# Kernel optimization log

Measured on AMD Instinct MI355X. Metric: run time of the kernel, lower is better.

Reference implementation:

```python
import jax, jax.numpy as jnp
import numpy as np

B, Tin, Tout = 256, 32, 29
Venc, Vdec = 29, 72
E = 256; H = 256; L = 3; G = 4 * H; D = 2 * L  # bidirectional dirs * layers


def lstm_step(x, h, c, Wih0, Wih1, Whh, b):
    """One timestep of a 3-layer bidirectional LSTM (torch gate order i,f,g,o).
    x: [B, in], h/c: [D, B, H] in torch layout (layer-major, dir-minor)."""
    new_h, new_c = [], []
    inp = x
    for l in range(L):
        outs = []
        for d in range(2):
            idx = 2 * l + d
            Wih = Wih0[d] if l == 0 else Wih1[l - 1, d]
            g = inp @ Wih.T + h[idx] @ Whh[l, d].T + b[l, d]
            i_g, f_g, g_g, o_g = jnp.split(g, 4, axis=-1)
            cc = jax.nn.sigmoid(f_g) * c[idx] + jax.nn.sigmoid(i_g) * jnp.tanh(g_g)
            hh = jax.nn.sigmoid(o_g) * jnp.tanh(cc)
            new_h.append(hh); new_c.append(cc); outs.append(hh)
        inp = jnp.concatenate(outs, axis=-1)  # feeds next layer: [B, 2H]
    return jnp.stack(new_h), jnp.stack(new_c), inp


def proj(hid, W1, b1, W2, b2):
    """Linear over hidden dim then Linear over the layer*dir dim -- the exact
    math of torch's linear1 -> permute(2,1,0) -> linear2 -> permute(2,1,0)."""
    hn = jnp.einsum('lbh,gh->lbg', hid, W1) + b1            # [D, B, H]
    return jnp.einsum('lbh,ml->mbh', hn, W2) + b2[:, None, None]


def setup_inputs() -> dict:
    key = jax.random.key(0)
    ks = iter(jax.random.split(key, 64))
    def p(shape, scale=0.06):
        return jax.random.normal(next(ks), shape, jnp.float32) * scale
    return {
        "input": jax.random.randint(next(ks), (B, Tin), 0, Venc),
        "target": jax.random.randint(next(ks), (B, Tout), 0, Vdec),
        "teacher_force": 1,
        "enc_emb": p((Venc, E)), "dec_emb": p((Vdec, E)),
        "enc_Wih0": p((2, G, E)), "enc_Wih1": p((L - 1, 2, G, 2 * H)),
        "enc_Whh": p((L, 2, G, H)), "enc_b": p((L, 2, G)),
        "dec_Wih0": p((2, G, E)), "dec_Wih1": p((L - 1, 2, G, 2 * H)),
        "dec_Whh": p((L, 2, G, H)), "dec_b": p((L, 2, G)),
        "lin_h_W1": p((H, H)), "lin_h_b1": p((H,)), "lin_h_W2": p((D, D)), "lin_h_b2": p((D,)),
        "lin_c_W1": p((H, H)), "lin_c_b1": p((H,)), "lin_c_W2": p((D, D)), "lin_c_b2": p((D,)),
        "lin_a_W1": p((H, H)), "lin_a_b1": p((H,)), "lin_a_W2": p((D, D)), "lin_a_b2": p((D,)),
        "attn_W": p((E, E + H)), "attn_b": p((E,)),
        "fc_W": p((Vdec, 2 * H)), "fc_b": p((Vdec,)),
    }


def reference(input, target, teacher_force, enc_emb, dec_emb, enc_Wih0, enc_Wih1, enc_Whh, enc_b, dec_Wih0, dec_Wih1, dec_Whh, dec_b, lin_h_W1, lin_h_b1, lin_h_W2, lin_h_b2, lin_c_W1, lin_c_b1, lin_c_W2, lin_c_b2, lin_a_W1, lin_a_b1, lin_a_W2, lin_a_b2, attn_W, attn_b, fc_W, fc_b):
    Bb = input.shape[0]
    h0 = jnp.zeros((D, Bb, H), jnp.float32)

    # ---- encoder: step LSTM over Tin, projecting hidden per step for attention ----
    def enc_step(carry, x_t):
        h, c = carry
        h, c, _ = lstm_step(enc_emb[x_t], h, c, enc_Wih0, enc_Wih1, enc_Whh, enc_b)
        return (h, c), proj(h, lin_a_W1, lin_a_b1, lin_a_W2, lin_a_b2)

    (h, c), encoder_outputs = jax.lax.scan(enc_step, (h0, h0), input.T)  # [Tin, D, B, H]

    # ---- encoder->decoder state bridging (linear over H, linear over D) ----
    dec_h = proj(h, lin_h_W1, lin_h_b1, lin_h_W2, lin_h_b2)
    dec_c = proj(c, lin_c_W1, lin_c_b1, lin_c_W2, lin_c_b2)

    def dec_core(h, c, tok):
        emb = dec_emb[tok]                                # [B, E]
        energies = h[None] * encoder_outputs              # [Tin, D, B, H]
        aw = jax.nn.softmax(energies, axis=0)             # attn over source time
        ctx = (aw * encoder_outputs).sum(0).mean(0)       # [B, H]
        x = jnp.concatenate([emb, ctx], -1) @ attn_W.T + attn_b
        h, c, top = lstm_step(x, h, c, dec_Wih0, dec_Wih1, dec_Whh, dec_b)
        return h, c, top @ fc_W.T + fc_b, aw.sum(-1)      # logits [B,V], aw [Tin,D,B]

    if teacher_force:
        def step(carry, tok):
            h, c = carry
            h, c, logits, _ = dec_core(h, c, tok)
            return (h, c), logits
        _, logits_seq = jax.lax.scan(step, (dec_h, dec_c), target[:, :Tout - 1].T)
        attn_seq = jnp.zeros((Tout - 1, Tin, D, Bb), jnp.float32)
    else:
        def step(carry, _):
            h, c, tok = carry
            h, c, logits, aw = dec_core(h, c, tok)
            nxt = jnp.argmax(jax.nn.softmax(logits, -1), -1).astype(tok.dtype)
            return (h, c, nxt), (logits, aw)
        tok0 = jnp.ones((Bb,), input.dtype)
        _, (logits_seq, attn_seq) = jax.lax.scan(step, (dec_h, dec_c, tok0), None, length=Tout - 1)

    pred0 = jnp.zeros((1, Bb, Vdec), jnp.float32).at[0, :, 1].set(1.0)
    predicted = jnp.concatenate([pred0, logits_seq], 0)   # [Tout, B, Vdec]
    attn_weights = jnp.concatenate([jnp.zeros((1, Tin, D, Bb), jnp.float32), attn_seq], 0)
    return predicted, attn_weights
```

## Files before the change

kernel.cpp:

```cpp
#include <hip/hip_runtime.h>
#include <math.h>

#define BB 256
#define TIN 32
#define TOUT 29
#define VDEC 72
#define EDIM 256
#define HDIM 256
#define DD 6
#define BH (BB*HDIM)
#define NBLK 256

typedef unsigned short u16;
typedef unsigned int u32;
typedef __bf16 bf16x8 __attribute__((ext_vector_type(8)));
typedef float f32x4 __attribute__((ext_vector_type(4)));
typedef u16 u16x8 __attribute__((ext_vector_type(8)));

__device__ __forceinline__ float sigmf(float x){ return 1.0f/(1.0f+__expf(-x)); }
__device__ __forceinline__ float tanhf_fast(float x){ return 1.0f - 2.0f/(1.0f+__expf(2.0f*x)); }
__device__ __forceinline__ u16 f2bf(float f){
  u32 u = __builtin_bit_cast(u32, f);
  u32 r = (u + 0x7fffu + ((u>>16)&1u)) >> 16;
  return (u16)r;
}
__device__ __forceinline__ float bf2f(u16 s){
  u32 u = ((u32)s)<<16; return __builtin_bit_cast(float, u);
}
__device__ __forceinline__ bf16x8 ldbf8(const u16* p){
  u16x8 t = *(const u16x8*)p; return __builtin_bit_cast(bf16x8, t);
}
__device__ __forceinline__ bf16x8 ldbf8v(const u16* p){
  u16x8 t = *(const volatile u16x8*)p; return __builtin_bit_cast(bf16x8, t);
}
__device__ __forceinline__ float ldbfv(const u16* p){ return bf2f(*(const volatile u16*)p); }
__device__ __forceinline__ float ldfv(const float* p){ return *(const volatile float*)p; }
__device__ __forceinline__ f32x4 mfma16(bf16x8 a, bf16x8 b, f32x4 c){
  return __builtin_amdgcn_mfma_f32_16x16x32_bf16(a, b, c, 0, 0, 0);
}

struct GmS { float As[32][33]; float Ws[256][34]; };
union SharedU {
  struct { float Gt[2][4][32][18]; } st;
  GmS gm2[2];
  struct { float s[512]; float p4[VDEC][4]; float lg[VDEC]; float ctxp[2][256]; int tok; } fc;
};

__device__ __forceinline__ void xbar(u32* barblk, int mt, u32 g, int bid, bool fast){
  __syncthreads();
  if (fast){
    u32* cnt  = barblk + 384 + mt*32;
    u32* genx = cnt + 16;
    if (threadIdx.x == 0){
      u32 old = __hip_atomic_fetch_add(cnt, 1u, __ATOMIC_RELAXED, __HIP_MEMORY_SCOPE_AGENT);
      if (old == 31u){
        __hip_atomic_store(cnt, 0u, __ATOMIC_RELAXED, __HIP_MEMORY_SCOPE_AGENT);
        __hip_atomic_store(genx, g, __ATOMIC_RELEASE, __HIP_MEMORY_SCOPE_AGENT);
      } else {
        while (__hip_atomic_load(genx, __ATOMIC_RELAXED, __HIP_MEMORY_SCOPE_AGENT) < g)
          __builtin_amdgcn_s_sleep(2);
      }
    }
    __syncthreads();
  } else {
    u32* arr = barblk;
    u32* gen = barblk + 320;
    if (threadIdx.x == 0)
      __hip_atomic_store(&arr[bid], g, __ATOMIC_RELEASE, __HIP_MEMORY_SCOPE_AGENT);
    if (bid == 0){
      if (threadIdx.x < 256)
        while (__hip_atomic_load(&arr[threadIdx.x], __ATOMIC_RELAXED, __HIP_MEMORY_SCOPE_AGENT) < g)
          __builtin_amdgcn_s_sleep(2);
      __syncthreads();
      if (threadIdx.x == 0)
        __hip_atomic_store(gen, g, __ATOMIC_RELEASE, __HIP_MEMORY_SCOPE_AGENT);
    } else if (threadIdx.x == 0){
      while (__hip_atomic_load(gen, __ATOMIC_RELAXED, __HIP_MEMORY_SCOPE_AGENT) < g)
        __builtin_amdgcn_s_sleep(2);
    }
    __builtin_amdgcn_fence(__ATOMIC_ACQUIRE, "agent");
    __syncthreads();
  }
}

__global__ void fill_zero_u32(u32* __restrict__ p, int n){
  int i = blockIdx.x*256 + threadIdx.x;
  if (i < n) p[i] = 0u;
}

__global__ void init_out_kernel(float* __restrict__ out, int n){
  int i = blockIdx.x*256 + threadIdx.x;
  if (i >= n) return;
  float v = 0.0f;
  if (i < BB*VDEC && (i % VDEC) == 1) v = 1.0f;
  out[i] = v;
}

__global__ void bias2d_kernel(const float* __restrict__ W2a, const float* __restrict__ b1a, const float* __restrict__ b2a,
                              const float* __restrict__ W2h, const float* __restrict__ b1h, const float* __restrict__ b2h,
                              const float* __restrict__ W2c, const float* __restrict__ b1c, const float* __restrict__ b2c,
                              float* __restrict__ outp){
  int g = threadIdx.x;
  const float* W2[3] = {W2a, W2h, W2c};
  const float* b1[3] = {b1a, b1h, b1c};
  const float* b2[3] = {b2a, b2h, b2c};
  for (int p = 0; p < 3; p++)
    for (int m = 0; m < 6; m++){
      float s = 0.f;
      for (int l = 0; l < 6; l++) s += W2[p][m*6+l];
      outp[p*1536 + m*256 + g] = s * b1[p][g] + b2[p][m];
    }
}

__global__ void embed_enc_kernel(const int* __restrict__ input, const float* __restrict__ enc_emb,
                                 u16* __restrict__ x_emb){
  int i = blockIdx.x*256 + threadIdx.x;
  int e = i & 255, b = (i >> 8) & 255, t = i >> 16;
  x_emb[i] = f2bf(enc_emb[(size_t)input[b*TIN + t]*EDIM + e]);
}

__global__ void pack_w_kernel(const float* __restrict__ Wih, const float* __restrict__ Whh,
                              u16* __restrict__ dst, int K1, int K){
  int k = blockIdx.x*256 + threadIdx.x;
  int row = blockIdx.y;
  int d = row >> 10, rr = row & 1023;
  int ht = rr >> 6, r = rr & 63;
  int g = (r>>4)*256 + ht*16 + (r&15);
  float v;
  if (k < K1) v = Wih[((size_t)d*1024 + g)*K1 + k];
  else        v = Whh[((size_t)d*1024 + g)*256 + (k - K1)];
  dst[(size_t)row*K + k] = f2bf(v);
}

__global__ void pack_wfused_kernel(const float* __restrict__ Wih0, const float* __restrict__ attn_W,
                                   const float* __restrict__ Whh, u16* __restrict__ dst){
  int k = blockIdx.x*256 + threadIdx.x;
  int row = blockIdx.y;
  int d = row >> 10, rr = row & 1023;
  int ht = rr >> 6, r = rr & 63;
  int g = (r>>4)*256 + ht*16 + (r&15);
  float v;
  if (k >= 512) v = Whh[((size_t)d*1024 + g)*256 + (k - 512)];
  else {
    const float* wr = Wih0 + ((size_t)d*1024 + g)*256;
    float s = 0.f;
    #pragma unroll 4
    for (int o = 0; o < 256; o++) s += wr[o] * attn_W[(size_t)o*512 + k];
    v = s;
  }
  dst[(size_t)row*768 + k] = f2bf(v);
}

__global__ void biasfold_kernel(const float* __restrict__ Wih0, const float* __restrict__ attn_b,
                                const float* __restrict__ dec_b, float* __restrict__ outb){
  int i = blockIdx.x*256 + threadIdx.x;
  int d = i >> 10, g = i & 1023;
  const float* wr = Wih0 + ((size_t)d*1024 + g)*256;
  float s = dec_b[d*1024 + g];
  #pragma unroll 4
  for (int o = 0; o < 256; o++) s += wr[o]*attn_b[o];
  outb[i] = s;
}

template<int K1>
__device__ __forceinline__ void stage_phase(SharedU* shp, int mt, int y,
    const u16* __restrict__ inp, const u16* __restrict__ Wpk, const float* __restrict__ bias_l,
    const u16* __restrict__ hR, u16* __restrict__ hW, float* __restrict__ cBuf,
    u16* __restrict__ inp_out, float* __restrict__ h_all_t, int l){
  auto& ss = shp->st;
  constexpr int K = K1 + 256;
  constexpr int HK = K/2;
  int tid = threadIdx.x;
  int m_base = mt*32;
  int d = y >> 4, ht = y & 15;
  int idx = 2*l + d;
  int q8 = tid >> 6, lane = tid & 63;
  int qg = q8 & 3, kh2 = q8 >> 2;
  int r = lane & 15, lq = lane >> 4;
  const u16* a0p = inp + (size_t)(m_base + r)*K1 + lq*8;
  const u16* a1p = a0p + (size_t)16*K1;
  const u16* h0p = hR + (size_t)idx*BH + (size_t)(m_base + r)*HDIM + lq*8;
  const u16* h1p = h0p + 16*HDIM;
  const u16* wp  = Wpk + (size_t)((d*16+ht)*64 + qg*16 + r)*K + lq*8;
  const int cbase = kh2*HK;
  f32x4 acc0 = {0.f,0.f,0.f,0.f}, acc1 = {0.f,0.f,0.f,0.f};
  #pragma unroll
  for (int c = 0; c < HK; c += 32){
    int col = cbase + c;
    bool ina = (col < K1);
    const u16* pa0 = ina ? (a0p + col) : (h0p + (col - K1));
    const u16* pa1 = ina ? (a1p + col) : (h1p + (col - K1));
    bf16x8 a0 = ldbf8v(pa0);
    bf16x8 a1 = ldbf8v(pa1);
    bf16x8 bq = ldbf8(wp + col);
    acc0 = mfma16(a0, bq, acc0);
    acc1 = mfma16(a1, bq, acc1);
  }
  __syncthreads();
  #pragma unroll
  for (int rr = 0; rr < 4; rr++){
    ss.Gt[kh2][qg][lq*4 + rr][r]      = acc0[rr];
    ss.Gt[kh2][qg][16 + lq*4 + rr][r] = acc1[rr];
  }
  __syncthreads();
  const float* bias = bias_l + d*1024;
  {
    int bb = tid >> 4, h2 = tid & 15;
    int b = m_base + bb, h = ht*16 + h2;
    float iv = ss.Gt[0][0][bb][h2] + ss.Gt[1][0][bb][h2] + bias[h];
    float fv = ss.Gt[0][1][bb][h2] + ss.Gt[1][1][bb][h2] + bias[256 + h];
    float gv = ss.Gt[0][2][bb][h2] + ss.Gt[1][2][bb][h2] + bias[512 + h];
    float ov = ss.Gt[0][3][bb][h2] + ss.Gt[1][3][bb][h2] + bias[768 + h];
    size_t off = (size_t)idx*BH + (size_t)b*HDIM + h;
    float cold = cBuf[off];
    float cc = sigmf(fv)*cold + sigmf(iv)*tanhf_fast(gv);
    float hv = sigmf(ov)*tanhf_fast(cc);
    cBuf[off] = cc;
    u16 hb = f2bf(hv);
    hW[off] = hb;
    if (inp_out) inp_out[(size_t)b*512 + d*HDIM + h] = hb;
    if (h_all_t) h_all_t[off] = hv;
  }
}

__device__ __forceinline__ void mix_one(int b, int h, const float* __restrict__ inp,
    float* __restrict__ outp, const float* __restrict__ W2, int t){
  size_t base2 = ((size_t)t*6)*BH + (size_t)b*256 + h;
  float v[6];
  #pragma unroll
  for (int l = 0; l < 6; l++) v[l] = ldfv(&inp[base2 + (size_t)l*BH]);
  #pragma unroll
  for (int m = 0; m < 6; m++){
    float s = 0.f;
    #pragma unroll
    for (int l = 0; l < 6; l++) s += W2[m*6+l]*v[l];
    outp[base2 + (size_t)m*BH] = s;
  }
}

__device__ __forceinline__ void gemm_tile(GmS& sg, int tid, int m_base,
    const float* __restrict__ A, float* __restrict__ C, const float* __restrict__ W,
    const float* __restrict__ bias2d, u16* __restrict__ Cbf){
  int rg = tid >> 5, cg = tid & 31;
  float acc[4][8];
  #pragma unroll
  for (int i=0;i<4;i++)
    #pragma unroll
    for (int j=0;j<8;j++) acc[i][j]=0.f;
  for (int k0 = 0; k0 < 256; k0 += 32){
    #pragma unroll
    for (int p=0;p<4;p++) sg.As[rg + p*8][cg] = ldfv(&A[(size_t)(m_base + rg + p*8)*256 + k0 + cg]);
    #pragma unroll
    for (int p=0;p<32;p++) sg.Ws[rg + p*8][cg] = W[(size_t)(rg + p*8)*256 + k0 + cg];
    __syncthreads();
    #pragma unroll
    for (int kk=0; kk<32; kk++){
      float a[4], w[8];
      #pragma unroll
      for (int i=0;i<4;i++) a[i] = sg.As[rg*4+i][kk];
      #pragma unroll
      for (int j=0;j<8;j++) w[j] = sg.Ws[cg + 32*j][kk];
      #pragma unroll
      for (int i=0;i<4;i++)
        #pragma unroll
        for (int j=0;j<8;j++) acc[i][j] += a[i]*w[j];
    }
    __syncthreads();
  }
  #pragma unroll
  for (int i=0;i<4;i++){
    int row = m_base + rg*4 + i;
    int bm = (row >> 8) % 6;
    #pragma unroll
    for (int j=0;j<8;j++){
      int col = cg + 32*j;
      float v = acc[i][j] + bias2d[bm*256 + col];
      if (C)   C[(size_t)row*256 + col] = v;
      if (Cbf) Cbf[(size_t)row*256 + col] = f2bf(v);
    }
  }
}

__device__ __forceinline__ void attn_phase(SharedU* shp, int b, int step,
    const u16* __restrict__ hR, const u16* __restrict__ eo, u16* __restrict__ cat,
    const int* __restrict__ tf, float* __restrict__ attn_out,
    const int* __restrict__ target, float* __restrict__ outp,
    const float* __restrict__ dec_emb, const u16* __restrict__ top,
    const float* __restrict__ fc_W, const float* __restrict__ fc_b){
  auto& sf = shp->fc;
  int tid = threadIdx.x;
  if (step > 0){
    sf.s[tid] = ldbfv(&top[(size_t)b*512 + tid]);
    __syncthreads();
    if (tid < 4*VDEC){
      int v = tid >> 2, part = tid & 3;
      int k0 = part*128;
      const float* wr = fc_W + (size_t)v*512;
      float a = 0.f;
      #pragma unroll 4
      for (int k = k0; k < k0+128; k++) a += sf.s[k]*wr[k];
      sf.p4[v][part] = a;
    }
    __syncthreads();
    if (tid < VDEC){
      float a = fc_b[tid] + sf.p4[tid][0] + sf.p4[tid][1] + sf.p4[tid][2] + sf.p4[tid][3];
      outp[((size_t)step*BB + b)*VDEC + tid] = a;
      sf.lg[tid] = a;
    }
    __syncthreads();
  }
  int tok;
  if (tf[0]) tok = target[b*TOUT + step];
  else if (step == 0) tok = 1;
  else {
    if (tid == 0){
      int bi = 0; float bv = sf.lg[0];
      for (int v = 1; v < VDEC; v++){ float x = sf.lg[v]; if (x > bv){ bv = x; bi = v; } }
      sf.tok = bi;
    }
    __syncthreads();
    tok = sf.tok;
  }
  if (tid < 256) cat[(size_t)b*512 + tid] = f2bf(dec_emb[(size_t)tok*EDIM + tid]);
  int hc = tid & 255, dhalf = tid >> 8;
  bool wa = (tf[0] == 0);
  float acc = 0.f;
  for (int dd = 0; dd < 3; dd++){
    int d = dhalf*3 + dd;
    float hv = ldbfv(&hR[(size_t)d*BH + (size_t)b*256 + hc]);
    const u16* ep = eo + (size_t)d*BH + (size_t)b*256 + hc;
    float se = 0.f, ac = 0.f;
    #pragma unroll 8
    for (int t = 0; t < TIN; t++){
      float ev = bf2f(ep[(size_t)t*(DD*BH)]);
      float e = __expf(hv*ev);
      se += e; ac += e*ev;
    }
    acc += ac/se;
    if (wa){
      float inv = 1.f/se;
      for (int t = 0; t < TIN; t++){
        float ev = bf2f(ep[(size_t)t*(DD*BH)]);
        atomicAdd(&attn_out[(((size_t)(step+1)*TIN + t)*DD + d)*BB + b], __expf(hv*ev)*inv);
      }
    }
  }
  sf.ctxp[dhalf][hc] = acc;
  __syncthreads();
  if (tid < 256)
    cat[(size_t)b*512 + 256 + tid] = f2bf((sf.ctxp[0][tid] + sf.ctxp[1][tid])*(1.0f/6.0f));
}

__device__ __forceinline__ void fc_final_phase(SharedU* shp, int b,
    const u16* __restrict__ top, const float* __restrict__ fc_W,
    const float* __restrict__ fc_b, float* __restrict__ outp){
  auto& sf = shp->fc;
  int tid = threadIdx.x;
  sf.s[tid] = ldbfv(&top[(size_t)b*512 + tid]);
  __syncthreads();
  if (tid < 4*VDEC){
    int v = tid >> 2, part = tid & 3;
    int k0 = part*128;
    const float* wr = fc_W + (size_t)v*512;
    float a = 0.f;
    #pragma unroll 4
    for (int k = k0; k < k0+128; k++) a += sf.s[k]*wr[k];
    sf.p4[v][part] = a;
  }
  __syncthreads();
  if (tid < VDEC){
    float a = fc_b[tid] + sf.p4[tid][0] + sf.p4[tid][1] + sf.p4[tid][2] + sf.p4[tid][3];
    outp[((size_t)(TOUT-1)*BB + b)*VDEC + tid] = a;
  }
}

__global__ __launch_bounds__(512, 2) void mega_kernel(
    const int* __restrict__ target, const int* __restrict__ tf,
    const float* __restrict__ dec_emb, const u16* __restrict__ x_emb,
    const u16* __restrict__ wp_e0, const u16* __restrict__ wp_e1, const u16* __restrict__ wp_e2,
    const u16* __restrict__ wp_d0f, const u16* __restrict__ wp_d1, const u16* __restrict__ wp_d2,
    const float* __restrict__ enc_b, const float* __restrict__ dec_b, const float* __restrict__ fb0,
    const float* __restrict__ lin_h_W1, const float* __restrict__ lin_c_W1, const float* __restrict__ lin_a_W1,
    const float* __restrict__ lin_h_W2, const float* __restrict__ lin_c_W2, const float* __restrict__ lin_a_W2,
    const float* __restrict__ bias2d,
    const float* __restrict__ fc_W, const float* __restrict__ fc_b,
    float* __restrict__ out,
    float* __restrict__ h_all, float* __restrict__ tmp6, float* __restrict__ tmp6c,
    float* __restrict__ dec_c, u16* __restrict__ enc_hA, float* __restrict__ enc_c,
    u16* __restrict__ enc_hB, u16* __restrict__ dec_hA, u16* __restrict__ dec_hB,
    u16* __restrict__ bufA, u16* __restrict__ bufB, u16* __restrict__ cat,
    u16* __restrict__ eo_bf, u32* __restrict__ barblk)
{
  __shared__ SharedU sh;
  __shared__ u32 ord_sh;
  const int bid = blockIdx.x, tid = threadIdx.x;
  u32* ctr = barblk + 336;
  u32* badflag = barblk + 352;
  u32 g = 0;

  u32 xcc;
  asm volatile("s_getreg_b32 %0, hwreg(HW_REG_XCC_ID)" : "=s"(xcc));
  xcc &= 7u;
  if (tid == 0){
    u32 o = __hip_atomic_fetch_add(&ctr[xcc], 1u, __ATOMIC_RELAXED, __HIP_MEMORY_SCOPE_AGENT);
    ord_sh = o;
    if (o >= 32u)
      __hip_atomic_store(badflag, 1u, __ATOMIC_RELAXED, __HIP_MEMORY_SCOPE_AGENT);
  }
  xbar(barblk, 0, ++g, bid, false);
  bool fast = (__hip_atomic_load(badflag, __ATOMIC_RELAXED, __HIP_MEMORY_SCOPE_AGENT) == 0u);
  int mt, y;
  if (fast){ mt = (int)xcc; y = (int)ord_sh; }
  else     { mt = bid & 7;  y = bid >> 3;    }
  const int half = tid >> 8, htid = tid & 255;
  const int b = mt*32 + y;

  for (int t = 0; t < TIN; t++){
    const u16* hRb = (t & 1) ? enc_hB : enc_hA;
    u16*       hWb = (t & 1) ? enc_hA : enc_hB;
    float* hat = h_all + (size_t)t*DD*BH;
    stage_phase<256>(&sh, mt, y, x_emb + (size_t)t*BB*EDIM, wp_e0, enc_b,        hRb, hWb, enc_c, bufA, hat, 0);
    xbar(barblk, mt, ++g, bid, fast);
    stage_phase<512>(&sh, mt, y, bufA,                      wp_e1, enc_b + 2048, hRb, hWb, enc_c, bufB, hat, 1);
    xbar(barblk, mt, ++g, bid, fast);
    stage_phase<512>(&sh, mt, y, bufB,                      wp_e2, enc_b + 4096, hRb, hWb, enc_c, nullptr, hat, 2);
  }
  xbar(barblk, mt, ++g, bid, fast);

  {
    if (half == 0) mix_one(b, htid, h_all + (size_t)31*DD*BH, tmp6,  lin_h_W2, 0);
    else           mix_one(b, htid, enc_c,                    tmp6c, lin_c_W2, 0);
    __syncthreads();
    for (int t2 = half*16; t2 < half*16 + 16; t2++)
      mix_one(b, htid, h_all, h_all, lin_a_W2, t2);
  }
  xbar(barblk, mt, ++g, bid, fast);
  if (y < 6){
    if (half == 0) gemm_tile(sh.gm2[0], htid, y*256 + mt*32, tmp6,  nullptr, lin_h_W1, bias2d + 1536, dec_hA);
    else           gemm_tile(sh.gm2[1], htid, y*256 + mt*32, tmp6c, dec_c,   lin_c_W1, bias2d + 3072, nullptr);
  }
  #pragma unroll
  for (int jj = 0; jj < 3; jj++){
    int k2 = y*6 + half*3 + jj;
    gemm_tile(sh.gm2[half], htid, k2*256 + mt*32, h_all, nullptr, lin_a_W1, bias2d, eo_bf);
  }
  xbar(barblk, mt, ++g, bid, fast);

  float* attn_out = out + (size_t)TOUT*BB*VDEC;
  for (int i = 0; i < TOUT-1; i++){
    const u16* hRb = (i & 1) ? dec_hB : dec_hA;
    u16*       hWb = (i & 1) ? dec_hA : dec_hB;
    attn_phase(&sh, b, i, hRb, eo_bf, cat, tf, attn_out, target, out, dec_emb, bufA, fc_W, fc_b);
    xbar(barblk, mt, ++g, bid, fast);
    stage_phase<512>(&sh, mt, y, cat,  wp_d0f, fb0,          hRb, hWb, dec_c, bufA, nullptr, 0);
    xbar(barblk, mt, ++g, bid, fast);
    stage_phase<512>(&sh, mt, y, bufA, wp_d1,  dec_b + 2048, hRb, hWb, dec_c, bufB, nullptr, 1);
    xbar(barblk, mt, ++g, bid, fast);
    stage_phase<512>(&sh, mt, y, bufB, wp_d2,  dec_b + 4096, hRb, hWb, dec_c, bufA, nullptr, 2);
    xbar(barblk, mt, ++g, bid, fast);
  }
  fc_final_phase(&sh, b, bufA, fc_W, fc_b, out);
}


extern "C" void kernel_launch(void* const* d_in, const int* in_sizes, int n_in,
                              void* d_out, int out_size, void* d_ws, size_t ws_size,
                              hipStream_t stream){
  (void)in_sizes; (void)n_in; (void)out_size; (void)ws_size;
  const int*   input    = (const int*)d_in[0];
  const int*   target   = (const int*)d_in[1];
  const int*   tf       = (const int*)d_in[2];
  const float* enc_emb  = (const float*)d_in[3];
  const float* dec_emb  = (const float*)d_in[4];
  const float* enc_Wih0 = (const float*)d_in[5];
  const float* enc_Wih1 = (const float*)d_in[6];
  const float* enc_Whh  = (const float*)d_in[7];
  const float* enc_b    = (const float*)d_in[8];
  const float* dec_Wih0 = (const float*)d_in[9];
  const float* dec_Wih1 = (const float*)d_in[10];
  const float* dec_Whh  = (const float*)d_in[11];
  const float* dec_b    = (const float*)d_in[12];
  const float* lin_h_W1 = (const float*)d_in[13];
  const float* lin_h_b1 = (const float*)d_in[14];
  const float* lin_h_W2 = (const float*)d_in[15];
  const float* lin_h_b2 = (const float*)d_in[16];
  const float* lin_c_W1 = (const float*)d_in[17];
  const float* lin_c_b1 = (const float*)d_in[18];
  const float* lin_c_W2 = (const float*)d_in[19];
  const float* lin_c_b2 = (const float*)d_in[20];
  const float* lin_a_W1 = (const float*)d_in[21];
  const float* lin_a_b1 = (const float*)d_in[22];
  const float* lin_a_W2 = (const float*)d_in[23];
  const float* lin_a_b2 = (const float*)d_in[24];
  const float* attn_W   = (const float*)d_in[25];
  const float* attn_b   = (const float*)d_in[26];
  const float* fc_W     = (const float*)d_in[27];
  const float* fc_b     = (const float*)d_in[28];
  float* out = (float*)d_out;

  char* base = (char*)d_ws;
  size_t off = 0;
  auto alloc = [&](size_t bytes)->char*{
    char* p = base + off; off += (bytes + 255) & ~(size_t)255; return p;
  };
  float* h_all  = (float*)alloc(sizeof(float)*(size_t)TIN*DD*BH);
  float* tmp6   = (float*)alloc(sizeof(float)*(size_t)DD*BH);
  float* tmp6c  = (float*)alloc(sizeof(float)*(size_t)DD*BH);
  float* dec_c  = (float*)alloc(sizeof(float)*(size_t)DD*BH);
  float* bias2d = (float*)alloc(sizeof(float)*3*6*256);
  u16*   enc_hA = (u16*)alloc(sizeof(u16)*(size_t)DD*BH + sizeof(float)*(size_t)DD*BH);
  float* enc_c  = (float*)(enc_hA + (size_t)DD*BH);
  u16* enc_hB = (u16*)alloc(sizeof(u16)*(size_t)DD*BH);
  u16* dec_hA = (u16*)alloc(sizeof(u16)*(size_t)DD*BH);
  u16* dec_hB = (u16*)alloc(sizeof(u16)*(size_t)DD*BH);
  u16* x_emb  = (u16*)alloc(sizeof(u16)*(size_t)TIN*BB*EDIM);
  u16* bufA   = (u16*)alloc(sizeof(u16)*(size_t)BB*512);
  u16* bufB   = (u16*)alloc(sizeof(u16)*(size_t)BB*512);
  u16* cat    = (u16*)alloc(sizeof(u16)*(size_t)BB*512);
  u16* eo_bf  = (u16*)alloc(sizeof(u16)*(size_t)TIN*DD*BH);
  u16* wp_e0  = (u16*)alloc(sizeof(u16)*(size_t)2048*512);
  u16* wp_e1  = (u16*)alloc(sizeof(u16)*(size_t)2048*768);
  u16* wp_e2  = (u16*)alloc(sizeof(u16)*(size_t)2048*768);
  u16* wp_d0f = (u16*)alloc(sizeof(u16)*(size_t)2048*768);
  u16* wp_d1  = (u16*)alloc(sizeof(u16)*(size_t)2048*768);
  u16* wp_d2  = (u16*)alloc(sizeof(u16)*(size_t)2048*768);
  float* fb0  = (float*)alloc(sizeof(float)*2048);
  u32* barblk = (u32*)alloc(sizeof(u32)*1024);

  const int outn = TOUT*BB*VDEC + TOUT*TIN*DD*BB;
  init_out_kernel<<<(outn+255)/256, 256, 0, stream>>>(out, outn);
  fill_zero_u32<<<(DD*BH*6/4 + 255)/256, 256, 0, stream>>>((u32*)enc_hA, DD*BH*6/4);
  fill_zero_u32<<<4, 256, 0, stream>>>(barblk, 1024);
  bias2d_kernel<<<1, 256, 0, stream>>>(lin_a_W2, lin_a_b1, lin_a_b2,
                                       lin_h_W2, lin_h_b1, lin_h_b2,
                                       lin_c_W2, lin_c_b1, lin_c_b2, bias2d);
  embed_enc_kernel<<<(TIN*BB*EDIM)/256, 256, 0, stream>>>(input, enc_emb, x_emb);
  pack_w_kernel<<<dim3(2,2048), 256, 0, stream>>>(enc_Wih0, enc_Whh,                       wp_e0, 256, 512);
  pack_w_kernel<<<dim3(3,2048), 256, 0, stream>>>(enc_Wih1, enc_Whh + 2*1024*256,          wp_e1, 512, 768);
  pack_w_kernel<<<dim3(3,2048), 256, 0, stream>>>(enc_Wih1 + (size_t)2*1024*512, enc_Whh + 4*1024*256, wp_e2, 512, 768);
  pack_wfused_kernel<<<dim3(3,2048), 256, 0, stream>>>(dec_Wih0, attn_W, dec_Whh,          wp_d0f);
  biasfold_kernel<<<8, 256, 0, stream>>>(dec_Wih0, attn_b, dec_b, fb0);
  pack_w_kernel<<<dim3(3,2048), 256, 0, stream>>>(dec_Wih1, dec_Whh + 2*1024*256,          wp_d1, 512, 768);
  pack_w_kernel<<<dim3(3,2048), 256, 0, stream>>>(dec_Wih1 + (size_t)2*1024*512, dec_Whh + 4*1024*256, wp_d2, 512, 768);

  mega_kernel<<<NBLK, 512, 0, stream>>>(
      target, tf, dec_emb, x_emb,
      wp_e0, wp_e1, wp_e2, wp_d0f, wp_d1, wp_d2,
      enc_b, dec_b, fb0,
      lin_h_W1, lin_c_W1, lin_a_W1, lin_h_W2, lin_c_W2, lin_a_W2,
      bias2d, fc_W, fc_b, out,
      h_all, tmp6, tmp6c, dec_c, enc_hA, enc_c, enc_hB, dec_hA, dec_hB,
      bufA, bufB, cat, eo_bf, barblk);
}
```

Measured before the change: 3.896 ms.

## Run encoder layers as per-block full-sequence passes with state kept in LDS

The encoder is restructured so that each of 32 worker blocks owns one direction and one 16-row batch tile and runs all 32 timesteps of a layer alone. The recurrent hidden state lives in shared memory and the cell state in registers. This replaces the roughly 96 grid-wide barriers per encoder pass with three layer-level barriers. The fast barrier is also rewritten to use a monotonic counter with no reset, and its sleep interval is shortened. The trade-off is that only 32 of 256 blocks do encoder work, and each re-streams its weight slice from L2 every timestep.

```diff
diff --git a/kernel.cpp b/kernel.cpp
--- a/kernel.cpp
+++ b/kernel.cpp
@@ -42,45 +42,45 @@
 struct GmS { float As[32][33]; float Ws[256][34]; };
 union SharedU {
   struct { float Gt[2][4][32][18]; } st;
+  struct { u16 hprev[16][264]; } enc;
   GmS gm2[2];
   struct { float s[512]; float p4[VDEC][4]; float lg[VDEC]; float ctxp[2][256]; int tok; } fc;
 };
 
-__device__ __forceinline__ void xbar(u32* barblk, int mt, u32 g, int bid, bool fast){
-  __syncthreads();
-  if (fast){
-    u32* cnt  = barblk + 384 + mt*32;
-    u32* genx = cnt + 16;
-    if (threadIdx.x == 0){
-      u32 old = __hip_atomic_fetch_add(cnt, 1u, __ATOMIC_RELAXED, __HIP_MEMORY_SCOPE_AGENT);
-      if (old == 31u){
-        __hip_atomic_store(cnt, 0u, __ATOMIC_RELAXED, __HIP_MEMORY_SCOPE_AGENT);
-        __hip_atomic_store(genx, g, __ATOMIC_RELEASE, __HIP_MEMORY_SCOPE_AGENT);
-      } else {
-        while (__hip_atomic_load(genx, __ATOMIC_RELAXED, __HIP_MEMORY_SCOPE_AGENT) < g)
-          __builtin_amdgcn_s_sleep(2);
-      }
-    }
-    __syncthreads();
-  } else {
-    u32* arr = barblk;
-    u32* gen = barblk + 320;
+__device__ __forceinline__ void bar_slow(u32* barblk, u32 gs, int bid){
+  __syncthreads();
+  u32* arr = barblk;
+  u32* gen = barblk + 320;
+  if (threadIdx.x == 0)
+    __hip_atomic_store(&arr[bid], gs, __ATOMIC_RELEASE, __HIP_MEMORY_SCOPE_AGENT);
+  if (bid == 0){
+    if (threadIdx.x < 256)
+      while (__hip_atomic_load(&arr[threadIdx.x], __ATOMIC_RELAXED, __HIP_MEMORY_SCOPE_AGENT) < gs)
+        __builtin_amdgcn_s_sleep(8);
+    __syncthreads();
     if (threadIdx.x == 0)
-      __hip_atomic_store(&arr[bid], g, __ATOMIC_RELEASE, __HIP_MEMORY_SCOPE_AGENT);
-    if (bid == 0){
-      if (threadIdx.x < 256)
-        while (__hip_atomic_load(&arr[threadIdx.x], __ATOMIC_RELAXED, __HIP_MEMORY_SCOPE_AGENT) < g)
-          __builtin_amdgcn_s_sleep(2);
-      __syncthreads();
-      if (threadIdx.x == 0)
-        __hip_atomic_store(gen, g, __ATOMIC_RELEASE, __HIP_MEMORY_SCOPE_AGENT);
-    } else if (threadIdx.x == 0){
-      while (__hip_atomic_load(gen, __ATOMIC_RELAXED, __HIP_MEMORY_SCOPE_AGENT) < g)
-        __builtin_amdgcn_s_sleep(2);
-    }
-    __builtin_amdgcn_fence(__ATOMIC_ACQUIRE, "agent");
-    __syncthreads();
-  }
+      __hip_atomic_store(gen, gs, __ATOMIC_RELEASE, __HIP_MEMORY_SCOPE_AGENT);
+  } else if (threadIdx.x == 0){
+    while (__hip_atomic_load(gen, __ATOMIC_RELAXED, __HIP_MEMORY_SCOPE_AGENT) < gs)
+      __builtin_amdgcn_s_sleep(8);
+  }
+  __builtin_amdgcn_fence(__ATOMIC_ACQUIRE, "agent");
+  __syncthreads();
+}
+
+__device__ __forceinline__ void bar_fast(u32* barblk, int mt, u32 gf){
+  __syncthreads();
+  u32* cnt  = barblk + 384 + mt*32;
+  u32* genx = cnt + 16;
+  if (threadIdx.x == 0){
+    u32 old = __hip_atomic_fetch_add(cnt, 1u, __ATOMIC_RELAXED, __HIP_MEMORY_SCOPE_AGENT);
+    if (old == gf*32u - 1u)
+      __hip_atomic_store(genx, gf, __ATOMIC_RELAXED, __HIP_MEMORY_SCOPE_AGENT);
+    else
+      while (__hip_atomic_load(genx, __ATOMIC_RELAXED, __HIP_MEMORY_SCOPE_AGENT) < gf)
+        __builtin_amdgcn_s_sleep(1);
+  }
+  __syncthreads();
 }
 
 __global__ void fill_zero_u32(u32* __restrict__ p, int n){
@@ -163,10 +163,81 @@
 }
 
 template<int K1>
-__device__ __forceinline__ void stage_phase(SharedU* shp, int mt, int y,
+__device__ __forceinline__ void enc_pass(SharedU* shp, int m0, int d,
+    const u16* __restrict__ g0, const u16* __restrict__ g1, size_t gtstride,
+    const u16* __restrict__ Wpk, const float* __restrict__ bias_d,
+    u16* __restrict__ hseq_p, float* __restrict__ hall_p, float* __restrict__ encc_p){
+  constexpr int K = K1 + 256;
+  const int tid = threadIdx.x;
+  const int wv = tid >> 6, lane = tid & 63;
+  const int r = lane & 15, lq = lane >> 4;
+  for (int i = tid; i < 16*264; i += 512) ((u16*)shp->enc.hprev)[i] = 0;
+  __syncthreads();
+  const u16* wrow[8];
+  #pragma unroll
+  for (int ht2 = 0; ht2 < 2; ht2++)
+    #pragma unroll
+    for (int q = 0; q < 4; q++)
+      wrow[ht2*4+q] = Wpk + (size_t)((d*16 + wv*2 + ht2)*64 + q*16 + r)*K + lq*8;
+  float c8[8];
+  #pragma unroll
+  for (int i = 0; i < 8; i++) c8[i] = 0.f;
+  const int mb = lq*4;
+  #pragma unroll 1
+  for (int t = 0; t < TIN; t++){
+    f32x4 acc[8];
+    #pragma unroll
+    for (int i = 0; i < 8; i++) acc[i] = (f32x4){0.f,0.f,0.f,0.f};
+    #pragma unroll
+    for (int k0 = 0; k0 < K; k0 += 32){
+      bf16x8 a;
+      if (k0 < K1){
+        const u16* gp = (K1 == 512 && k0 >= 256) ? g1 : g0;
+        a = ldbf8v(gp + (size_t)t*gtstride + (size_t)(m0 + r)*256 + (k0 & 255) + lq*8);
+      } else {
+        a = ldbf8(&shp->enc.hprev[r][(k0 - K1) + lq*8]);
+      }
+      #pragma unroll
+      for (int i = 0; i < 8; i++)
+        acc[i] = mfma16(a, ldbf8(wrow[i] + k0), acc[i]);
+    }
+    __syncthreads();
+    #pragma unroll
+    for (int ht2 = 0; ht2 < 2; ht2++){
+      int h = (wv*2 + ht2)*16 + r;
+      #pragma unroll
+      for (int reg = 0; reg < 4; reg++){
+        float iv = acc[ht2*4+0][reg] + bias_d[h];
+        float fv = acc[ht2*4+1][reg] + bias_d[256 + h];
+        float gv = acc[ht2*4+2][reg] + bias_d[512 + h];
+        float ov = acc[ht2*4+3][reg] + bias_d[768 + h];
+        float co = c8[ht2*4+reg];
+        float cc = sigmf(fv)*co + sigmf(iv)*tanhf_fast(gv);
+        float hv = sigmf(ov)*tanhf_fast(cc);
+        c8[ht2*4+reg] = cc;
+        u16 hb = f2bf(hv);
+        shp->enc.hprev[mb + reg][h] = hb;
+        size_t go = (size_t)(m0 + mb + reg)*256 + h;
+        hseq_p[(size_t)t*(DD*BH) + go] = hb;
+        hall_p[(size_t)t*(DD*BH) + go] = hv;
+      }
+    }
+    __syncthreads();
+  }
+  #pragma unroll
+  for (int ht2 = 0; ht2 < 2; ht2++){
+    int h = (wv*2 + ht2)*16 + r;
+    #pragma unroll
+    for (int reg = 0; reg < 4; reg++)
+      encc_p[(size_t)(m0 + mb + reg)*256 + h] = c8[ht2*4+reg];
+  }
+}
+
+template<int K1>
+__device__ __forceinline__ void stage_dec(SharedU* shp, int mt, int y,
     const u16* __restrict__ inp, const u16* __restrict__ Wpk, const float* __restrict__ bias_l,
     const u16* __restrict__ hR, u16* __restrict__ hW, float* __restrict__ cBuf,
-    u16* __restrict__ inp_out, float* __restrict__ h_all_t, int l){
+    u16* __restrict__ inp_out, int l){
   auto& ss = shp->st;
   constexpr int K = K1 + 256;
   constexpr int HK = K/2;
@@ -203,8 +274,8 @@
     ss.Gt[kh2][qg][16 + lq*4 + rr][r] = acc1[rr];
   }
   __syncthreads();
-  const float* bias = bias_l + d*1024;
   {
+    const float* bias = bias_l + d*1024;
     int bb = tid >> 4, h2 = tid & 15;
     int b = m_base + bb, h = ht*16 + h2;
     float iv = ss.Gt[0][0][bb][h2] + ss.Gt[1][0][bb][h2] + bias[h];
@@ -219,7 +290,6 @@
     u16 hb = f2bf(hv);
     hW[off] = hb;
     if (inp_out) inp_out[(size_t)b*512 + d*HDIM + h] = hb;
-    if (h_all_t) h_all_t[off] = hv;
   }
 }
 
@@ -386,8 +456,8 @@
     const float* __restrict__ fc_W, const float* __restrict__ fc_b,
     float* __restrict__ out,
     float* __restrict__ h_all, float* __restrict__ tmp6, float* __restrict__ tmp6c,
-    float* __restrict__ dec_c, u16* __restrict__ enc_hA, float* __restrict__ enc_c,
-    u16* __restrict__ enc_hB, u16* __restrict__ dec_hA, u16* __restrict__ dec_hB,
+    float* __restrict__ dec_c, float* __restrict__ enc_c,
+    u16* __restrict__ hseq, u16* __restrict__ dec_hA, u16* __restrict__ dec_hB,
     u16* __restrict__ bufA, u16* __restrict__ bufB, u16* __restrict__ cat,
     u16* __restrict__ eo_bf, u32* __restrict__ barblk)
 {
@@ -396,7 +466,7 @@
   const int bid = blockIdx.x, tid = threadIdx.x;
   u32* ctr = barblk + 336;
   u32* badflag = barblk + 352;
-  u32 g = 0;
+  u32 gs = 0, gf = 0;
 
   u32 xcc;
   asm volatile("s_getreg_b32 %0, hwreg(HW_REG_XCC_ID)" : "=s"(xcc));
@@ -407,7 +477,7 @@
     if (o >= 32u)
       __hip_atomic_store(badflag, 1u, __ATOMIC_RELAXED, __HIP_MEMORY_SCOPE_AGENT);
   }
-  xbar(barblk, 0, ++g, bid, false);
+  ++gs; bar_slow(barblk, gs, bid);
   bool fast = (__hip_atomic_load(badflag, __ATOMIC_RELAXED, __HIP_MEMORY_SCOPE_AGENT) == 0u);
   int mt, y;
   if (fast){ mt = (int)xcc; y = (int)ord_sh; }
@@ -415,17 +485,25 @@
   const int half = tid >> 8, htid = tid & 255;
   const int b = mt*32 + y;
 
-  for (int t = 0; t < TIN; t++){
-    const u16* hRb = (t & 1) ? enc_hB : enc_hA;
-    u16*       hWb = (t & 1) ? enc_hA : enc_hB;
-    float* hat = h_all + (size_t)t*DD*BH;
-    stage_phase<256>(&sh, mt, y, x_emb + (size_t)t*BB*EDIM, wp_e0, enc_b,        hRb, hWb, enc_c, bufA, hat, 0);
-    xbar(barblk, mt, ++g, bid, fast);
-    stage_phase<512>(&sh, mt, y, bufA,                      wp_e1, enc_b + 2048, hRb, hWb, enc_c, bufB, hat, 1);
-    xbar(barblk, mt, ++g, bid, fast);
-    stage_phase<512>(&sh, mt, y, bufB,                      wp_e2, enc_b + 4096, hRb, hWb, enc_c, nullptr, hat, 2);
-  }
-  xbar(barblk, mt, ++g, bid, fast);
+  bool worker; int wdir, wtile;
+  if (fast){ worker = (y < 4); wdir = mt >> 2; wtile = (mt & 3)*4 + y; }
+  else     { worker = (bid < 32); wdir = bid >> 4; wtile = bid & 15; }
+  const int m0 = wtile*16;
+
+  if (worker)
+    enc_pass<256>(&sh, m0, wdir, x_emb, x_emb, (size_t)BH, wp_e0, enc_b + wdir*1024,
+                  hseq + (size_t)(0+wdir)*BH, h_all + (size_t)(0+wdir)*BH, enc_c + (size_t)(0+wdir)*BH);
+  ++gs; bar_slow(barblk, gs, bid);
+  if (worker)
+    enc_pass<512>(&sh, m0, wdir, hseq + 0*(size_t)BH, hseq + 1*(size_t)BH, (size_t)(DD*BH),
+                  wp_e1, enc_b + 2048 + wdir*1024,
+                  hseq + (size_t)(2+wdir)*BH, h_all + (size_t)(2+wdir)*BH, enc_c + (size_t)(2+wdir)*BH);
+  ++gs; bar_slow(barblk, gs, bid);
+  if (worker)
+    enc_pass<512>(&sh, m0, wdir, hseq + 2*(size_t)BH, hseq + 3*(size_t)BH, (size_t)(DD*BH),
+                  wp_e2, enc_b + 4096 + wdir*1024,
+                  hseq + (size_t)(4+wdir)*BH, h_all + (size_t)(4+wdir)*BH, enc_c + (size_t)(4+wdir)*BH);
+  ++gs; bar_slow(barblk, gs, bid);
 
   {
     if (half == 0) mix_one(b, htid, h_all + (size_t)31*DD*BH, tmp6,  lin_h_W2, 0);
@@ -434,7 +512,7 @@
     for (int t2 = half*16; t2 < half*16 + 16; t2++)
       mix_one(b, htid, h_all, h_all, lin_a_W2, t2);
   }
-  xbar(barblk, mt, ++g, bid, fast);
+  if (fast){ ++gf; bar_fast(barblk, mt, gf); } else { ++gs; bar_slow(barblk, gs, bid); }
   if (y < 6){
     if (half == 0) gemm_tile(sh.gm2[0], htid, y*256 + mt*32, tmp6,  nullptr, lin_h_W1, bias2d + 1536, dec_hA);
     else           gemm_tile(sh.gm2[1], htid, y*256 + mt*32, tmp6c, dec_c,   lin_c_W1, bias2d + 3072, nullptr);
@@ -444,20 +522,20 @@
     int k2 = y*6 + half*3 + jj;
     gemm_tile(sh.gm2[half], htid, k2*256 + mt*32, h_all, nullptr, lin_a_W1, bias2d, eo_bf);
   }
-  xbar(barblk, mt, ++g, bid, fast);
+  if (fast){ ++gf; bar_fast(barblk, mt, gf); } else { ++gs; bar_slow(barblk, gs, bid); }
 
   float* attn_out = out + (size_t)TOUT*BB*VDEC;
   for (int i = 0; i < TOUT-1; i++){
     const u16* hRb = (i & 1) ? dec_hB : dec_hA;
     u16*       hWb = (i & 1) ? dec_hA : dec_hB;
     attn_phase(&sh, b, i, hRb, eo_bf, cat, tf, attn_out, target, out, dec_emb, bufA, fc_W, fc_b);
-    xbar(barblk, mt, ++g, bid, fast);
-    stage_phase<512>(&sh, mt, y, cat,  wp_d0f, fb0,          hRb, hWb, dec_c, bufA, nullptr, 0);
-    xbar(barblk, mt, ++g, bid, fast);
-    stage_phase<512>(&sh, mt, y, bufA, wp_d1,  dec_b + 2048, hRb, hWb, dec_c, bufB, nullptr, 1);
-    xbar(barblk, mt, ++g, bid, fast);
-    stage_phase<512>(&sh, mt, y, bufB, wp_d2,  dec_b + 4096, hRb, hWb, dec_c, bufA, nullptr, 2);
-    xbar(barblk, mt, ++g, bid, fast);
+    if (fast){ ++gf; bar_fast(barblk, mt, gf); } else { ++gs; bar_slow(barblk, gs, bid); }
+    stage_dec<512>(&sh, mt, y, cat,  wp_d0f, fb0,          hRb, hWb, dec_c, bufA, 0);
+    if (fast){ ++gf; bar_fast(barblk, mt, gf); } else { ++gs; bar_slow(barblk, gs, bid); }
+    stage_dec<512>(&sh, mt, y, bufA, wp_d1,  dec_b + 2048, hRb, hWb, dec_c, bufB, 1);
+    if (fast){ ++gf; bar_fast(barblk, mt, gf); } else { ++gs; bar_slow(barblk, gs, bid); }
+    stage_dec<512>(&sh, mt, y, bufB, wp_d2,  dec_b + 4096, hRb, hWb, dec_c, bufA, 2);
+    if (fast){ ++gf; bar_fast(barblk, mt, gf); } else { ++gs; bar_slow(barblk, gs, bid); }
   }
   fc_final_phase(&sh, b, bufA, fc_W, fc_b, out);
 }
@@ -508,9 +586,8 @@
   float* tmp6c  = (float*)alloc(sizeof(float)*(size_t)DD*BH);
   float* dec_c  = (float*)alloc(sizeof(float)*(size_t)DD*BH);
   float* bias2d = (float*)alloc(sizeof(float)*3*6*256);
-  u16*   enc_hA = (u16*)alloc(sizeof(u16)*(size_t)DD*BH + sizeof(float)*(size_t)DD*BH);
-  float* enc_c  = (float*)(enc_hA + (size_t)DD*BH);
-  u16* enc_hB = (u16*)alloc(sizeof(u16)*(size_t)DD*BH);
+  float* enc_c  = (float*)alloc(sizeof(float)*(size_t)DD*BH);
+  u16* hseq   = (u16*)alloc(sizeof(u16)*(size_t)TIN*DD*BH);
   u16* dec_hA = (u16*)alloc(sizeof(u16)*(size_t)DD*BH);
   u16* dec_hB = (u16*)alloc(sizeof(u16)*(size_t)DD*BH);
   u16* x_emb  = (u16*)alloc(sizeof(u16)*(size_t)TIN*BB*EDIM);
@@ -529,7 +606,6 @@
 
   const int outn = TOUT*BB*VDEC + TOUT*TIN*DD*BB;
   init_out_kernel<<<(outn+255)/256, 256, 0, stream>>>(out, outn);
-  fill_zero_u32<<<(DD*BH*6/4 + 255)/256, 256, 0, stream>>>((u32*)enc_hA, DD*BH*6/4);
   fill_zero_u32<<<4, 256, 0, stream>>>(barblk, 1024);
   bias2d_kernel<<<1, 256, 0, stream>>>(lin_a_W2, lin_a_b1, lin_a_b2,
                                        lin_h_W2, lin_h_b1, lin_h_b2,
@@ -549,6 +625,6 @@
       enc_b, dec_b, fb0,
       lin_h_W1, lin_c_W1, lin_a_W1, lin_h_W2, lin_c_W2, lin_a_W2,
       bias2d, fc_W, fc_b, out,
-      h_all, tmp6, tmp6c, dec_c, enc_hA, enc_c, enc_hB, dec_hA, dec_hB,
+      h_all, tmp6, tmp6c, dec_c, enc_c, hseq, dec_hA, dec_hB,
       bufA, bufB, cat, eo_bf, barblk);
 }
```

Result: slower. 7.226 ms (+85.5%).
